# Kernel optimization log

Hardware: AMD Instinct MI355X
Metric: run time of the kernel (lower is better)

## Reference

```python
import jax, jax.numpy as jnp
import numpy as np

D = 32      # d_shape (internal width, also propagate_dimensions and out_channels)
S = 3       # space_dimensions
K = 40      # kNN neighbors
EPS = 1e-5  # BatchNorm1d eps


def _elu(x):
    return jax.nn.elu(x)


def _batchnorm(x, gamma, beta):
    # training-mode BatchNorm1d over all nodes (flattened batch*nodes), biased var
    mu = x.mean(axis=(0, 1))
    var = x.var(axis=(0, 1))
    return gamma * (x - mu) / jnp.sqrt(var + EPS) + beta


def _knn_mean_max(s, h):
    # s: [N, S] learned coords, h: [N, D] propagated features (one graph)
    N = s.shape[0]
    n2 = jnp.sum(s * s, axis=-1)                     # [N]
    d2 = n2[:, None] + n2[None, :] - 2.0 * (s @ s.T)  # [N, N] squared dists
    d2 = jnp.maximum(d2, 0.0)
    d2 = jnp.where(jnp.eye(N, dtype=bool), jnp.inf, d2)  # exclude self loops
    _, idx = jax.lax.top_k(-d2, K)                   # idx: [N, K] neighbor (src) ids per dst
    d2_sel = jnp.take_along_axis(d2, idx, axis=1)    # [N, K]
    pot = jnp.exp(-d2_sel)                           # gaussian potential exp(-||ds||^2)
    msg = pot[..., None] * h[idx]                    # [N, K, D] edge messages
    return jnp.concatenate([msg.mean(axis=1), msg.max(axis=1)], axis=-1)  # [N, 2D]


def setup_inputs() -> dict:
    key = jax.random.key(0)
    ks = jax.random.split(key, 12)
    B, N, C = 2, 8192, 9

    def lin_w(k, i, o):
        return (jax.random.normal(k, (i, o), jnp.float32) / np.sqrt(i)).astype(jnp.float32)

    return {
        "x": jax.random.normal(ks[0], (B, N, C), jnp.float32),
        # pre_gravnet: Linear(C->32), ELU, Linear(32->32), ELU
        "pre_W1": lin_w(ks[1], C, D), "pre_b1": jnp.zeros((D,), jnp.float32),
        "pre_W2": lin_w(ks[2], D, D), "pre_b2": jnp.zeros((D,), jnp.float32),
        "bn1_g": jnp.ones((D,), jnp.float32), "bn1_b": jnp.zeros((D,), jnp.float32),
        # GravNetConv: lin_s (no bias), lin_h, lin (in = D + 2D -> D)
        "lin_s_W": lin_w(ks[3], D, S),
        "lin_h_W": lin_w(ks[4], D, D), "lin_h_b": jnp.zeros((D,), jnp.float32),
        "lin_W": lin_w(ks[5], D + 2 * D, D), "lin_b": jnp.zeros((D,), jnp.float32),
        # post_gravnet: Linear(D+S+D -> 32), ELU, Linear(32->32), ELU
        "post_W1": lin_w(ks[6], D + S + D, D), "post_b1": jnp.zeros((D,), jnp.float32),
        "post_W2": lin_w(ks[7], D, D), "post_b2": jnp.zeros((D,), jnp.float32),
        "bn2_g": jnp.ones((D,), jnp.float32), "bn2_b": jnp.zeros((D,), jnp.float32),
    }


def reference(x, pre_W1, pre_b1, pre_W2, pre_b2, bn1_g, bn1_b,
              lin_s_W, lin_h_W, lin_h_b, lin_W, lin_b,
              post_W1, post_b1, post_W2, post_b2, bn2_g, bn2_b):
    # pre_gravnet MLP + batchnorm
    x1 = _elu(_elu(x @ pre_W1 + pre_b1) @ pre_W2 + pre_b2)
    x1 = _batchnorm(x1, bn1_g, bn1_b)

    # GravNetConv
    h_l = x1 @ lin_h_W + lin_h_b     # [B, N, D]
    s_l = x1 @ lin_s_W               # [B, N, S] learned coords
    agg = jax.vmap(_knn_mean_max)(s_l, h_l)           # [B, N, 2D]
    xgn = jnp.concatenate([agg, x1], axis=-1) @ lin_W + lin_b  # [B, N, D]

    # post_gravnet MLP + batchnorm
    xc = jnp.concatenate([xgn, s_l, x1], axis=-1)     # [B, N, D+S+D]
    out = _elu(_elu(xc @ post_W1 + post_b1) @ post_W2 + post_b2)
    out = _batchnorm(out, bn2_g, bn2_b)
    return out
```

## Files before the change

kernel.cpp:

```cpp
#include <hip/hip_runtime.h>
#include <math.h>

#define NN    8192
#define NODES 16384
#define KK    40
#define CAP   256


__device__ __forceinline__ float r13_elu(float x){ return x > 0.f ? x : expm1f(x); }

__device__ __forceinline__ unsigned r13_key(float4 si, float4 sj){
  float dot = si.x*sj.x + si.y*sj.y + si.z*sj.z;
  float d2 = si.w + sj.w - 2.0f*dot;
  d2 = fmaxf(d2, 0.0f);
  return __float_as_uint(d2);
}

__global__ __launch_bounds__(256) void r13_pre(const float* __restrict__ x,
    const float* __restrict__ W1, const float* __restrict__ b1,
    const float* __restrict__ W2, const float* __restrict__ b2,
    float* __restrict__ xpre, float* __restrict__ part1)
{
  __shared__ float sW1[9*32], sb1[32], sW2[32*32], sb2[32];
  __shared__ float wls[4][32], wls2[4][32];
  int t = threadIdx.x;
  for (int i = t; i < 9*32;  i += 256) sW1[i] = W1[i];
  for (int i = t; i < 32*32; i += 256) sW2[i] = W2[i];
  if (t < 32) { sb1[t] = b1[t]; sb2[t] = b2[t]; }
  __syncthreads();
  int node = blockIdx.x*256 + t;
  float xv[9], a1[32], a2[32];
  #pragma unroll
  for (int i=0;i<9;i++) xv[i] = x[node*9+i];
  #pragma unroll
  for (int o=0;o<32;o++){
    float a = sb1[o];
    #pragma unroll
    for (int i=0;i<9;i++) a += xv[i]*sW1[i*32+o];
    a1[o] = r13_elu(a);
  }
  #pragma unroll
  for (int o=0;o<32;o++){
    float a = sb2[o];
    #pragma unroll
    for (int i=0;i<32;i++) a += a1[i]*sW2[i*32+o];
    a2[o] = r13_elu(a);
    xpre[(size_t)node*32+o] = a2[o];
  }
  int lane = t & 63, w = t >> 6;
  #pragma unroll
  for (int c=0;c<32;c++){
    float v = a2[c], v2 = a2[c]*a2[c];
    #pragma unroll
    for (int off=32; off; off>>=1){ v += __shfl_down(v,(unsigned)off,64); v2 += __shfl_down(v2,(unsigned)off,64); }
    if (lane==0){ wls[w][c]=v; wls2[w][c]=v2; }
  }
  __syncthreads();
  if (t < 32){
    part1[blockIdx.x*64 + t]      = wls[0][t]+wls[1][t]+wls[2][t]+wls[3][t];
    part1[blockIdx.x*64 + 32 + t] = wls2[0][t]+wls2[1][t]+wls2[2][t]+wls2[3][t];
  }
}

__global__ __launch_bounds__(256) void r13_bnproj(const float* __restrict__ part1,
    const float* __restrict__ xpre,
    const float* __restrict__ bng, const float* __restrict__ bnb,
    const float* __restrict__ hW, const float* __restrict__ hb, const float* __restrict__ sW,
    float* __restrict__ x1, float* __restrict__ h, float4* __restrict__ s4)
{
  __shared__ float sHW[32*32], sHB[32], sSW[32*3];
  __shared__ float sstat[64];
  __shared__ float smu[32], sdev[32], sg[32], sbt[32];
  int t = threadIdx.x;
  for (int i=t;i<1024;i+=256) sHW[i]=hW[i];
  if (t < 96) sSW[t]=sW[t];
  if (t < 64){
    float s = 0.f;
    for (int b2=0;b2<64;b2++) s += part1[b2*64+t];
    sstat[t] = s;
  }
  __syncthreads();
  if (t < 32){
    sHB[t]=hb[t];
    float s = sstat[t], sq = sstat[32+t];
    float mu = s * (1.f/NODES);
    float var = sq * (1.f/NODES) - mu*mu;
    smu[t]=mu; sdev[t]=sqrtf(var+1e-5f);
    sg[t]=bng[t]; sbt[t]=bnb[t];
  }
  __syncthreads();
  int node = blockIdx.x*256+t;
  float v[32];
  #pragma unroll
  for (int c=0;c<32;c++){
    float a = xpre[(size_t)node*32+c];
    v[c] = sg[c]*(a - smu[c])/sdev[c] + sbt[c];
    x1[(size_t)node*32+c] = v[c];
  }
  #pragma unroll
  for (int o=0;o<32;o++){
    float a = sHB[o];
    #pragma unroll
    for (int i=0;i<32;i++) a += v[i]*sHW[i*32+o];
    h[(size_t)node*32+o] = a;
  }
  float s0=0.f,s1=0.f,s2=0.f;
  #pragma unroll
  for (int i=0;i<32;i++){
    s0 += v[i]*sSW[i*3+0];
    s1 += v[i]*sSW[i*3+1];
    s2 += v[i]*sSW[i*3+2];
  }
  float n2 = s0*s0 + s1*s1 + s2*s2;
  s4[node] = make_float4(s0,s1,s2,n2);
}

__global__ __launch_bounds__(256) void r13_knn(const float4* __restrict__ s4,
    const float* __restrict__ h, float* __restrict__ agg)
{
  __shared__ unsigned short binv[8192];
  __shared__ unsigned hist[1024];
  __shared__ int      sel[KK];
  __shared__ unsigned selk[KK];
  __shared__ float    pots[KK];
  __shared__ unsigned wsum[4], wtot[4];
  __shared__ unsigned sB1, sL1, candCount;

  int t = threadIdx.x;
  int lane = t & 63, w = t >> 6;
  int b = blockIdx.x >> 13;
  int i = blockIdx.x & (NN-1);
  const float4* sb = s4 + (size_t)b*NN;
  float4 si = sb[i];

  #pragma unroll
  for (int z=0; z<4; ++z) hist[z*256 + t] = 0u;
  if (t == 0) candCount = 0u;
  __syncthreads();

  #pragma unroll 4
  for (int c=0;c<32;c++){
    int j = c*256 + t;
    unsigned k = r13_key(si, sb[j]);
    if (j == i) k = 0x7F800000u;
    unsigned bin = k >> 21;
    binv[j] = (unsigned short)bin;
    atomicAdd(&hist[bin], 1u);
  }
  __syncthreads();

  unsigned c0 = hist[4*t+0], c1 = hist[4*t+1], c2 = hist[4*t+2], c3 = hist[4*t+3];
  unsigned chunk = c0+c1+c2+c3;
  unsigned sc = chunk;
  #pragma unroll
  for (int off=1; off<64; off<<=1){
    unsigned o = __shfl_up(sc, (unsigned)off, 64);
    if (lane >= off) sc += o;
  }
  if (lane == 63) wsum[w] = sc;
  __syncthreads();
  unsigned base = 0;
  for (int w2=0; w2<w; ++w2) base += wsum[w2];
  unsigned excl = base + sc - chunk;
  if (excl < KK && KK <= excl + chunk){
    unsigned acc = excl; int bb = 4*t;
    if (acc + c0 >= KK){ sB1 = (unsigned)bb;   sL1 = acc; }
    else { acc += c0;
      if (acc + c1 >= KK){ sB1 = (unsigned)(bb+1); sL1 = acc; }
      else { acc += c1;
        if (acc + c2 >= KK){ sB1 = (unsigned)(bb+2); sL1 = acc; }
        else { acc += c2;    sB1 = (unsigned)(bb+3); sL1 = acc; } } }
  }
  __syncthreads();
  unsigned B1 = sB1, L1 = sL1;
  unsigned* candk = &hist[0];
  unsigned* candj = &hist[CAP];

  unsigned lessmask = 0, bmask = 0; unsigned cnt = 0;
  #pragma unroll 4
  for (int c=0;c<32;c++){
    unsigned bin = binv[c*256+t];
    if (bin < B1){ lessmask |= 1u<<c; cnt++; }
    else if (bin == B1) bmask |= 1u<<c;
  }
  unsigned v = cnt;
  #pragma unroll
  for (int off=1; off<64; off<<=1){
    unsigned o = __shfl_up(v, (unsigned)off, 64);
    if (lane >= off) v += o;
  }
  if (lane == 63) wtot[w] = v;
  __syncthreads();
  unsigned gbase = 0;
  for (int w2=0; w2<w; ++w2) gbase += wtot[w2];
  unsigned offs = gbase + v - cnt;
  for (int c=0;c<32;c++){
    int j = c*256+t;
    if ((lessmask>>c)&1u){ sel[offs] = j; offs++; }
    else if ((bmask>>c)&1u){
      unsigned k = r13_key(si, sb[j]);
      unsigned slot = atomicAdd(&candCount, 1u);
      if (slot < CAP){ candk[slot] = k; candj[slot] = (unsigned)j; }
    }
  }
  __syncthreads();

  unsigned C1 = candCount; if (C1 > CAP) C1 = CAP;
  for (unsigned idx = (unsigned)t; idx < C1; idx += 256){
    unsigned k = candk[idx], j = candj[idx];
    unsigned rank = L1;
    for (unsigned u=0; u<C1; ++u){
      unsigned ku = candk[u], ju = candj[u];
      rank += (ku < k || (ku == k && ju < j)) ? 1u : 0u;
    }
    if (rank < KK){ sel[rank] = (int)j; selk[rank] = k; }
  }
  __syncthreads();
  if (t < (int)L1) selk[t] = r13_key(si, sb[sel[t]]);
  __syncthreads();

  if (t < KK) pots[t] = expf(-__uint_as_float(selk[t]));
  __syncthreads();
  float (*psum)[32] = (float(*)[32])&hist[512];
  float (*pmax)[32] = (float(*)[32])&hist[768];
  int ch = t & 31, g = t >> 5;
  const float* hb2 = h + (size_t)b*NN*32;
  float sum = 0.f, mx = -INFINITY;
  #pragma unroll
  for (int q=0;q<5;q++){
    int k2 = g*5 + q;
    float m = pots[k2] * hb2[(size_t)sel[k2]*32 + ch];
    sum += m; mx = fmaxf(mx, m);
  }
  psum[g][ch] = sum; pmax[g][ch] = mx;
  __syncthreads();
  if (t < 32){
    float s = 0.f, m2 = -INFINITY;
    #pragma unroll
    for (int g2=0;g2<8;g2++){ s += psum[g2][t]; m2 = fmaxf(m2, pmax[g2][t]); }
    float* ab = agg + (size_t)blockIdx.x*64;
    ab[t]    = s / 40.0f;
    ab[32+t] = m2;
  }
}

__global__ __launch_bounds__(256) void r13_post(const float* __restrict__ agg,
    const float* __restrict__ x1, const float4* __restrict__ s4,
    const float* __restrict__ linW, const float* __restrict__ linb,
    const float* __restrict__ pW1, const float* __restrict__ pb1,
    const float* __restrict__ pW2, const float* __restrict__ pb2,
    float* __restrict__ outpre, float* __restrict__ part2)
{
  __shared__ float sLW[96*32], sPW1[67*32], sPW2[32*32];
  __shared__ float sLB[32], sPB1[32], sPB2[32];
  __shared__ float wls[4][32], wls2[4][32];
  int t = threadIdx.x;
  for (int i=t;i<96*32;i+=256) sLW[i]=linW[i];
  for (int i=t;i<67*32;i+=256) sPW1[i]=pW1[i];
  for (int i=t;i<32*32;i+=256) sPW2[i]=pW2[i];
  if (t<32){ sLB[t]=linb[t]; sPB1[t]=pb1[t]; sPB2[t]=pb2[t]; }
  __syncthreads();
  int node = blockIdx.x*256+t;
  float av[64], xv[32];
  #pragma unroll
  for (int i=0;i<64;i++) av[i]=agg[(size_t)node*64+i];
  #pragma unroll
  for (int i=0;i<32;i++) xv[i]=x1[(size_t)node*32+i];
  float4 sv = s4[node];
  float xgn[32];
  #pragma unroll
  for (int o=0;o<32;o++){
    float a = sLB[o];
    #pragma unroll
    for (int i=0;i<64;i++) a += av[i]*sLW[i*32+o];
    #pragma unroll
    for (int i=0;i<32;i++) a += xv[i]*sLW[(64+i)*32+o];
    xgn[o]=a;
  }
  float p1[32];
  #pragma unroll
  for (int o=0;o<32;o++){
    float a = sPB1[o];
    #pragma unroll
    for (int i=0;i<32;i++) a += xgn[i]*sPW1[i*32+o];
    a += sv.x*sPW1[32*32+o] + sv.y*sPW1[33*32+o] + sv.z*sPW1[34*32+o];
    #pragma unroll
    for (int i=0;i<32;i++) a += xv[i]*sPW1[(35+i)*32+o];
    p1[o]=r13_elu(a);
  }
  float p2[32];
  #pragma unroll
  for (int o=0;o<32;o++){
    float a = sPB2[o];
    #pragma unroll
    for (int i=0;i<32;i++) a += p1[i]*sPW2[i*32+o];
    p2[o] = r13_elu(a);
    outpre[(size_t)node*32+o] = p2[o];
  }
  int lane = t & 63, w = t >> 6;
  #pragma unroll
  for (int c=0;c<32;c++){
    float v = p2[c], v2 = p2[c]*p2[c];
    #pragma unroll
    for (int off=32; off; off>>=1){ v += __shfl_down(v,(unsigned)off,64); v2 += __shfl_down(v2,(unsigned)off,64); }
    if (lane==0){ wls[w][c]=v; wls2[w][c]=v2; }
  }
  __syncthreads();
  if (t < 32){
    part2[blockIdx.x*64 + t]      = wls[0][t]+wls[1][t]+wls[2][t]+wls[3][t];
    part2[blockIdx.x*64 + 32 + t] = wls2[0][t]+wls2[1][t]+wls2[2][t]+wls2[3][t];
  }
}

__global__ __launch_bounds__(256) void r13_bnout(const float* __restrict__ part2,
    const float* __restrict__ outpre,
    const float* __restrict__ g, const float* __restrict__ b,
    float* __restrict__ out)
{
  __shared__ float sstat[64];
  __shared__ float smu[32], sdev2[32], sg2[32], sb2[32];
  int t = threadIdx.x;
  if (t < 64){
    float s = 0.f;
    for (int b2=0;b2<64;b2++) s += part2[b2*64+t];
    sstat[t] = s;
  }
  __syncthreads();
  if (t < 32){
    float s = sstat[t], sq = sstat[32+t];
    float mu = s * (1.f/NODES);
    float var = sq*(1.f/NODES) - mu*mu;
    smu[t] = mu; sdev2[t] = sqrtf(var+1e-5f);
    sg2[t] = g[t]; sb2[t] = b[t];
  }
  __syncthreads();
  int idx = blockIdx.x*256 + t;
  int c = idx & 31;
  out[idx] = sg2[c]*(outpre[idx]-smu[c])/sdev2[c] + sb2[c];
}

extern "C" void kernel_launch(void* const* d_in, const int* in_sizes, int n_in,
                              void* d_out, int out_size, void* d_ws, size_t ws_size,
                              hipStream_t stream)
{
  (void)in_sizes; (void)n_in; (void)out_size; (void)ws_size;
  const float* x      = (const float*)d_in[0];
  const float* preW1  = (const float*)d_in[1];
  const float* preb1  = (const float*)d_in[2];
  const float* preW2  = (const float*)d_in[3];
  const float* preb2  = (const float*)d_in[4];
  const float* bn1g   = (const float*)d_in[5];
  const float* bn1b   = (const float*)d_in[6];
  const float* linsW  = (const float*)d_in[7];
  const float* linhW  = (const float*)d_in[8];
  const float* linhb  = (const float*)d_in[9];
  const float* linW   = (const float*)d_in[10];
  const float* linb   = (const float*)d_in[11];
  const float* postW1 = (const float*)d_in[12];
  const float* postb1 = (const float*)d_in[13];
  const float* postW2 = (const float*)d_in[14];
  const float* postb2 = (const float*)d_in[15];
  const float* bn2g   = (const float*)d_in[16];
  const float* bn2b   = (const float*)d_in[17];

  float* ws = (float*)d_ws;
  float* xpre   = ws;
  float* x1     = xpre   + (size_t)NODES*32;
  float* h      = x1     + (size_t)NODES*32;
  float* s4     = h      + (size_t)NODES*32;
  float* agg    = s4     + (size_t)NODES*4;
  float* outpre = agg    + (size_t)NODES*64;
  float* part1  = outpre + (size_t)NODES*32;
  float* part2  = part1  + 64*64;

  hipLaunchKernelGGL(r13_pre,    dim3(64),    dim3(256), 0, stream, x, preW1, preb1, preW2, preb2, xpre, part1);
  hipLaunchKernelGGL(r13_bnproj, dim3(64),    dim3(256), 0, stream, part1, xpre, bn1g, bn1b, linhW, linhb, linsW, x1, h, (float4*)s4);
  hipLaunchKernelGGL(r13_knn,    dim3(16384), dim3(256), 0, stream, (const float4*)s4, h, agg);
  hipLaunchKernelGGL(r13_post,   dim3(64),    dim3(256), 0, stream, agg, x1, (const float4*)s4, linW, linb, postW1, postb1, postW2, postb2, outpre, part2);
  hipLaunchKernelGGL(r13_bnout,  dim3(2048),  dim3(256), 0, stream, part2, outpre, bn2g, bn2b, (float*)d_out);
}
```

Baseline: 253.6 us.

## Process four query nodes per kNN block, recomputing distance keys instead of storing bins

The kNN kernel now handles four destination nodes per block, so each candidate coordinate load feeds four distance computations and four histograms. The per-node shared bin array is dropped and keys are recomputed in the second pass, trading extra ALU work for far less LDS. The grid shrinks fourfold. Scan, rank and aggregation steps are serialized per query with extra barriers, and register pressure rises.

```diff
diff --git a/kernel.cpp b/kernel.cpp
--- a/kernel.cpp
+++ b/kernel.cpp
@@ -7,16 +7,16 @@
 #define CAP   256
 
 
-__device__ __forceinline__ float r13_elu(float x){ return x > 0.f ? x : expm1f(x); }
-
-__device__ __forceinline__ unsigned r13_key(float4 si, float4 sj){
+__device__ __forceinline__ float r15_elu(float x){ return x > 0.f ? x : expm1f(x); }
+
+__device__ __forceinline__ unsigned r15_key(float4 si, float4 sj){
   float dot = si.x*sj.x + si.y*sj.y + si.z*sj.z;
   float d2 = si.w + sj.w - 2.0f*dot;
   d2 = fmaxf(d2, 0.0f);
   return __float_as_uint(d2);
 }
 
-__global__ __launch_bounds__(256) void r13_pre(const float* __restrict__ x,
+__global__ __launch_bounds__(256) void r15_pre(const float* __restrict__ x,
     const float* __restrict__ W1, const float* __restrict__ b1,
     const float* __restrict__ W2, const float* __restrict__ b2,
     float* __restrict__ xpre, float* __restrict__ part1)
@@ -37,14 +37,14 @@
     float a = sb1[o];
     #pragma unroll
     for (int i=0;i<9;i++) a += xv[i]*sW1[i*32+o];
-    a1[o] = r13_elu(a);
+    a1[o] = r15_elu(a);
   }
   #pragma unroll
   for (int o=0;o<32;o++){
     float a = sb2[o];
     #pragma unroll
     for (int i=0;i<32;i++) a += a1[i]*sW2[i*32+o];
-    a2[o] = r13_elu(a);
+    a2[o] = r15_elu(a);
     xpre[(size_t)node*32+o] = a2[o];
   }
   int lane = t & 63, w = t >> 6;
@@ -62,7 +62,7 @@
   }
 }
 
-__global__ __launch_bounds__(256) void r13_bnproj(const float* __restrict__ part1,
+__global__ __launch_bounds__(256) void r15_bnproj(const float* __restrict__ part1,
     const float* __restrict__ xpre,
     const float* __restrict__ bng, const float* __restrict__ bnb,
     const float* __restrict__ hW, const float* __restrict__ hb, const float* __restrict__ sW,
@@ -115,136 +115,172 @@
   s4[node] = make_float4(s0,s1,s2,n2);
 }
 
-__global__ __launch_bounds__(256) void r13_knn(const float4* __restrict__ s4,
+__global__ __launch_bounds__(256) void r15_knn(const float4* __restrict__ s4,
     const float* __restrict__ h, float* __restrict__ agg)
 {
-  __shared__ unsigned short binv[8192];
-  __shared__ unsigned hist[1024];
-  __shared__ int      sel[KK];
-  __shared__ unsigned selk[KK];
-  __shared__ float    pots[KK];
-  __shared__ unsigned wsum[4], wtot[4];
-  __shared__ unsigned sB1, sL1, candCount;
+  __shared__ unsigned hist[4][1024];
+  __shared__ int      sel[4][KK];
+  __shared__ unsigned selk[4][KK];
+  __shared__ float    pots[4][KK];
+  __shared__ unsigned wsum[4];
+  __shared__ unsigned wtot[4][4];
+  __shared__ unsigned sB1[4], sL1[4], candCount[4];
 
   int t = threadIdx.x;
   int lane = t & 63, w = t >> 6;
-  int b = blockIdx.x >> 13;
-  int i = blockIdx.x & (NN-1);
+  int b  = blockIdx.x >> 11;
+  int i0 = (blockIdx.x & 2047) * 4;
   const float4* sb = s4 + (size_t)b*NN;
-  float4 si = sb[i];
-
-  #pragma unroll
-  for (int z=0; z<4; ++z) hist[z*256 + t] = 0u;
-  if (t == 0) candCount = 0u;
-  __syncthreads();
-
-  #pragma unroll 4
+  float4 si[4]; int iq[4];
+  #pragma unroll
+  for (int q=0;q<4;q++){ iq[q] = i0+q; si[q] = sb[i0+q]; }
+
+  unsigned* histf = (unsigned*)hist;
+  #pragma unroll
+  for (int z=0; z<16; ++z) histf[z*256 + t] = 0u;
+  if (t < 4) candCount[t] = 0u;
+  __syncthreads();
+
+  #pragma unroll 2
   for (int c=0;c<32;c++){
     int j = c*256 + t;
-    unsigned k = r13_key(si, sb[j]);
-    if (j == i) k = 0x7F800000u;
-    unsigned bin = k >> 21;
-    binv[j] = (unsigned short)bin;
-    atomicAdd(&hist[bin], 1u);
-  }
-  __syncthreads();
-
-  unsigned c0 = hist[4*t+0], c1 = hist[4*t+1], c2 = hist[4*t+2], c3 = hist[4*t+3];
-  unsigned chunk = c0+c1+c2+c3;
-  unsigned sc = chunk;
-  #pragma unroll
-  for (int off=1; off<64; off<<=1){
-    unsigned o = __shfl_up(sc, (unsigned)off, 64);
-    if (lane >= off) sc += o;
-  }
-  if (lane == 63) wsum[w] = sc;
-  __syncthreads();
-  unsigned base = 0;
-  for (int w2=0; w2<w; ++w2) base += wsum[w2];
-  unsigned excl = base + sc - chunk;
-  if (excl < KK && KK <= excl + chunk){
-    unsigned acc = excl; int bb = 4*t;
-    if (acc + c0 >= KK){ sB1 = (unsigned)bb;   sL1 = acc; }
-    else { acc += c0;
-      if (acc + c1 >= KK){ sB1 = (unsigned)(bb+1); sL1 = acc; }
-      else { acc += c1;
-        if (acc + c2 >= KK){ sB1 = (unsigned)(bb+2); sL1 = acc; }
-        else { acc += c2;    sB1 = (unsigned)(bb+3); sL1 = acc; } } }
-  }
-  __syncthreads();
-  unsigned B1 = sB1, L1 = sL1;
-  unsigned* candk = &hist[0];
-  unsigned* candj = &hist[CAP];
-
-  unsigned lessmask = 0, bmask = 0; unsigned cnt = 0;
-  #pragma unroll 4
+    float4 sj = sb[j];
+    #pragma unroll
+    for (int q=0;q<4;q++){
+      unsigned k = r15_key(si[q], sj);
+      if (j == iq[q]) k = 0x7F800000u;
+      atomicAdd(&hist[q][k>>21], 1u);
+    }
+  }
+  __syncthreads();
+
+  for (int q=0;q<4;q++){
+    unsigned c0 = hist[q][4*t+0], c1 = hist[q][4*t+1], c2 = hist[q][4*t+2], c3 = hist[q][4*t+3];
+    unsigned chunk = c0+c1+c2+c3;
+    unsigned sc = chunk;
+    #pragma unroll
+    for (int off=1; off<64; off<<=1){
+      unsigned o = __shfl_up(sc, (unsigned)off, 64);
+      if (lane >= off) sc += o;
+    }
+    if (lane == 63) wsum[w] = sc;
+    __syncthreads();
+    unsigned base = 0;
+    for (int w2=0; w2<w; ++w2) base += wsum[w2];
+    unsigned excl = base + sc - chunk;
+    if (excl < KK && KK <= excl + chunk){
+      unsigned acc = excl; int bb = 4*t;
+      if (acc + c0 >= KK){ sB1[q] = (unsigned)bb;   sL1[q] = acc; }
+      else { acc += c0;
+        if (acc + c1 >= KK){ sB1[q] = (unsigned)(bb+1); sL1[q] = acc; }
+        else { acc += c1;
+          if (acc + c2 >= KK){ sB1[q] = (unsigned)(bb+2); sL1[q] = acc; }
+          else { acc += c2;    sB1[q] = (unsigned)(bb+3); sL1[q] = acc; } } }
+    }
+    __syncthreads();
+  }
+  unsigned B1r[4];
+  #pragma unroll
+  for (int q=0;q<4;q++) B1r[q] = sB1[q];
+  unsigned* candk = &histf[0];
+  unsigned* candj = &histf[1024];
+
+  unsigned lessm[4] = {0,0,0,0};
+  unsigned cnt[4]   = {0,0,0,0};
+  #pragma unroll 2
   for (int c=0;c<32;c++){
-    unsigned bin = binv[c*256+t];
-    if (bin < B1){ lessmask |= 1u<<c; cnt++; }
-    else if (bin == B1) bmask |= 1u<<c;
-  }
-  unsigned v = cnt;
-  #pragma unroll
-  for (int off=1; off<64; off<<=1){
-    unsigned o = __shfl_up(v, (unsigned)off, 64);
-    if (lane >= off) v += o;
-  }
-  if (lane == 63) wtot[w] = v;
-  __syncthreads();
-  unsigned gbase = 0;
-  for (int w2=0; w2<w; ++w2) gbase += wtot[w2];
-  unsigned offs = gbase + v - cnt;
-  for (int c=0;c<32;c++){
-    int j = c*256+t;
-    if ((lessmask>>c)&1u){ sel[offs] = j; offs++; }
-    else if ((bmask>>c)&1u){
-      unsigned k = r13_key(si, sb[j]);
-      unsigned slot = atomicAdd(&candCount, 1u);
-      if (slot < CAP){ candk[slot] = k; candj[slot] = (unsigned)j; }
-    }
-  }
-  __syncthreads();
-
-  unsigned C1 = candCount; if (C1 > CAP) C1 = CAP;
-  for (unsigned idx = (unsigned)t; idx < C1; idx += 256){
-    unsigned k = candk[idx], j = candj[idx];
-    unsigned rank = L1;
-    for (unsigned u=0; u<C1; ++u){
-      unsigned ku = candk[u], ju = candj[u];
-      rank += (ku < k || (ku == k && ju < j)) ? 1u : 0u;
-    }
-    if (rank < KK){ sel[rank] = (int)j; selk[rank] = k; }
-  }
-  __syncthreads();
-  if (t < (int)L1) selk[t] = r13_key(si, sb[sel[t]]);
-  __syncthreads();
-
-  if (t < KK) pots[t] = expf(-__uint_as_float(selk[t]));
-  __syncthreads();
-  float (*psum)[32] = (float(*)[32])&hist[512];
-  float (*pmax)[32] = (float(*)[32])&hist[768];
+    int j = c*256 + t;
+    float4 sj = sb[j];
+    #pragma unroll
+    for (int q=0;q<4;q++){
+      unsigned k = r15_key(si[q], sj);
+      if (j == iq[q]) k = 0x7F800000u;
+      unsigned bin = k >> 21;
+      if (bin < B1r[q]){ lessm[q] |= 1u<<c; cnt[q]++; }
+      else if (bin == B1r[q]){
+        unsigned slot = atomicAdd(&candCount[q], 1u);
+        if (slot < CAP){ candk[q*CAP+slot] = k; candj[q*CAP+slot] = (unsigned)j; }
+      }
+    }
+  }
+  unsigned vq[4];
+  #pragma unroll
+  for (int q=0;q<4;q++){
+    unsigned v = cnt[q];
+    #pragma unroll
+    for (int off=1; off<64; off<<=1){
+      unsigned o = __shfl_up(v, (unsigned)off, 64);
+      if (lane >= off) v += o;
+    }
+    if (lane == 63) wtot[q][w] = v;
+    vq[q] = v;
+  }
+  __syncthreads();
+  #pragma unroll
+  for (int q=0;q<4;q++){
+    unsigned gbase = 0;
+    for (int w2=0; w2<w; ++w2) gbase += wtot[q][w2];
+    unsigned offs = gbase + vq[q] - cnt[q];
+    unsigned m = lessm[q];
+    while (m){
+      int c = __builtin_ctz(m); m &= m-1u;
+      sel[q][offs++] = c*256 + t;
+    }
+  }
+  __syncthreads();
+
+  for (int q=0;q<4;q++){
+    unsigned C1 = candCount[q]; if (C1 > CAP) C1 = CAP;
+    unsigned L1 = sL1[q];
+    for (unsigned idx = (unsigned)t; idx < C1; idx += 256){
+      unsigned k = candk[q*CAP+idx], j = candj[q*CAP+idx];
+      unsigned rank = L1;
+      for (unsigned u=0; u<C1; ++u){
+        unsigned ku = candk[q*CAP+u], ju = candj[q*CAP+u];
+        rank += (ku < k || (ku == k && ju < j)) ? 1u : 0u;
+      }
+      if (rank < KK){ sel[q][rank] = (int)j; selk[q][rank] = k; }
+    }
+  }
+  __syncthreads();
+  #pragma unroll
+  for (int q=0;q<4;q++){
+    if (t < (int)sL1[q]) selk[q][t] = r15_key(si[q], sb[sel[q][t]]);
+  }
+  __syncthreads();
+  if (t < KK){
+    #pragma unroll
+    for (int q=0;q<4;q++) pots[q][t] = expf(-__uint_as_float(selk[q][t]));
+  }
+  __syncthreads();
+
+  float (*psum)[32] = (float(*)[32])&histf[2048];
+  float (*pmax)[32] = (float(*)[32])&histf[2304];
   int ch = t & 31, g = t >> 5;
   const float* hb2 = h + (size_t)b*NN*32;
-  float sum = 0.f, mx = -INFINITY;
-  #pragma unroll
-  for (int q=0;q<5;q++){
-    int k2 = g*5 + q;
-    float m = pots[k2] * hb2[(size_t)sel[k2]*32 + ch];
-    sum += m; mx = fmaxf(mx, m);
-  }
-  psum[g][ch] = sum; pmax[g][ch] = mx;
-  __syncthreads();
-  if (t < 32){
-    float s = 0.f, m2 = -INFINITY;
-    #pragma unroll
-    for (int g2=0;g2<8;g2++){ s += psum[g2][t]; m2 = fmaxf(m2, pmax[g2][t]); }
-    float* ab = agg + (size_t)blockIdx.x*64;
-    ab[t]    = s / 40.0f;
-    ab[32+t] = m2;
-  }
-}
-
-__global__ __launch_bounds__(256) void r13_post(const float* __restrict__ agg,
+  for (int q=0;q<4;q++){
+    float sum = 0.f, mx = -INFINITY;
+    #pragma unroll
+    for (int p=0;p<5;p++){
+      int k2 = g*5 + p;
+      float m = pots[q][k2] * hb2[(size_t)sel[q][k2]*32 + ch];
+      sum += m; mx = fmaxf(mx, m);
+    }
+    psum[g][ch] = sum; pmax[g][ch] = mx;
+    __syncthreads();
+    if (t < 32){
+      float s = 0.f, m2 = -INFINITY;
+      #pragma unroll
+      for (int g2=0;g2<8;g2++){ s += psum[g2][t]; m2 = fmaxf(m2, pmax[g2][t]); }
+      float* ab = agg + (size_t)(b*NN + i0 + q)*64;
+      ab[t]    = s / 40.0f;
+      ab[32+t] = m2;
+    }
+    __syncthreads();
+  }
+}
+
+__global__ __launch_bounds__(256) void r15_post(const float* __restrict__ agg,
     const float* __restrict__ x1, const float4* __restrict__ s4,
     const float* __restrict__ linW, const float* __restrict__ linb,
     const float* __restrict__ pW1, const float* __restrict__ pb1,
@@ -286,7 +322,7 @@
     a += sv.x*sPW1[32*32+o] + sv.y*sPW1[33*32+o] + sv.z*sPW1[34*32+o];
     #pragma unroll
     for (int i=0;i<32;i++) a += xv[i]*sPW1[(35+i)*32+o];
-    p1[o]=r13_elu(a);
+    p1[o]=r15_elu(a);
   }
   float p2[32];
   #pragma unroll
@@ -294,7 +330,7 @@
     float a = sPB2[o];
     #pragma unroll
     for (int i=0;i<32;i++) a += p1[i]*sPW2[i*32+o];
-    p2[o] = r13_elu(a);
+    p2[o] = r15_elu(a);
     outpre[(size_t)node*32+o] = p2[o];
   }
   int lane = t & 63, w = t >> 6;
@@ -312,7 +348,7 @@
   }
 }
 
-__global__ __launch_bounds__(256) void r13_bnout(const float* __restrict__ part2,
+__global__ __launch_bounds__(256) void r15_bnout(const float* __restrict__ part2,
     const float* __restrict__ outpre,
     const float* __restrict__ g, const float* __restrict__ b,
     float* __restrict__ out)
@@ -373,9 +409,9 @@
   float* part1  = outpre + (size_t)NODES*32;
   float* part2  = part1  + 64*64;
 
-  hipLaunchKernelGGL(r13_pre,    dim3(64),    dim3(256), 0, stream, x, preW1, preb1, preW2, preb2, xpre, part1);
-  hipLaunchKernelGGL(r13_bnproj, dim3(64),    dim3(256), 0, stream, part1, xpre, bn1g, bn1b, linhW, linhb, linsW, x1, h, (float4*)s4);
-  hipLaunchKernelGGL(r13_knn,    dim3(16384), dim3(256), 0, stream, (const float4*)s4, h, agg);
-  hipLaunchKernelGGL(r13_post,   dim3(64),    dim3(256), 0, stream, agg, x1, (const float4*)s4, linW, linb, postW1, postb1, postW2, postb2, outpre, part2);
-  hipLaunchKernelGGL(r13_bnout,  dim3(2048),  dim3(256), 0, stream, part2, outpre, bn2g, bn2b, (float*)d_out);
-}
+  hipLaunchKernelGGL(r15_pre,    dim3(64),    dim3(256), 0, stream, x, preW1, preb1, preW2, preb2, xpre, part1);
+  hipLaunchKernelGGL(r15_bnproj, dim3(64),    dim3(256), 0, stream, part1, xpre, bn1g, bn1b, linhW, linhb, linsW, x1, h, (float4*)s4);
+  hipLaunchKernelGGL(r15_knn,    dim3(4096),  dim3(256), 0, stream, (const float4*)s4, h, agg);
+  hipLaunchKernelGGL(r15_post,   dim3(64),    dim3(256), 0, stream, agg, x1, (const float4*)s4, linW, linb, postW1, postb1, postW2, postb2, outpre, part2);
+  hipLaunchKernelGGL(r15_bnout,  dim3(2048),  dim3(256), 0, stream, part2, outpre, bn2g, bn2b, (float*)d_out);
+}
```

Result: faster. 233.4 us (-8.0%).
